# Optimization experiments

Hardware: AMD Instinct MI355X
Metric: run time of the kernel (lower is better)

## Reference

```python
import jax, jax.numpy as jnp
import numpy as np

N = 100000   # nodes
E = 50000    # hyperedges
K = 4        # nodes per hyperedge
D = 128      # out_dim (= in_dim here)
ED = 64      # edge_dim
H = 8        # num_heads


def _build_pairs(seed=0):
    # Sparse equivalent of the incidence-matrix nested loops:
    # for each edge e with member set S, emit ordered pairs (v, e, u) for v,u in S.
    rng = np.random.default_rng(seed)
    cover = rng.permutation(N).reshape(N // K, K)          # guarantees every node owns >=1 pair group
    rand = rng.integers(0, N, size=(E - N // K, K))
    edge_nodes = np.concatenate([cover, rand], axis=0)      # [E, K]
    owners = np.repeat(edge_nodes, K, axis=1).ravel()       # v, repeated K times per edge slot
    pair_u = np.tile(edge_nodes, (1, K)).ravel()            # u, tiled
    pair_e = np.repeat(np.arange(E), K * K)
    return owners.astype(np.int32), pair_e.astype(np.int32), pair_u.astype(np.int32)


def setup_inputs() -> dict:
    key = jax.random.key(0)
    ks = jax.random.split(key, 12)
    owners, pair_e, pair_u = _build_pairs()
    s = 0.05
    return {
        "x": jax.random.normal(ks[0], (N, D), jnp.float32),
        "edge_attr": jax.random.normal(ks[1], (E, ED), jnp.float32),
        "w_lin": jax.random.normal(ks[2], (D, D), jnp.float32) * s,   # self.lin (no bias)
        "w_e": jax.random.normal(ks[3], (ED, D), jnp.float32) * s,    # self.edge_lin (no bias)
        "w_q": jax.random.normal(ks[4], (D, D), jnp.float32) * s,
        "b_q": jax.random.normal(ks[5], (D,), jnp.float32) * s,
        "w_k": jax.random.normal(ks[6], (D, D), jnp.float32) * s,
        "b_k": jax.random.normal(ks[7], (D,), jnp.float32) * s,
        "w_v": jax.random.normal(ks[8], (D, D), jnp.float32) * s,
        "b_v": jax.random.normal(ks[9], (D,), jnp.float32) * s,
        "w_o": jax.random.normal(ks[10], (D, D), jnp.float32) * s,
        "b_o": jax.random.normal(ks[11], (D,), jnp.float32) * s,
        "owners": jnp.asarray(owners),
        "pair_e": jnp.asarray(pair_e),
        "pair_u": jnp.asarray(pair_u),
    }


def reference(x, edge_attr, w_lin, w_e, w_q, b_q, w_k, b_k, w_v, b_v, w_o, b_o, owners, pair_e, pair_u):
    n = x.shape[0]
    d = w_lin.shape[1]
    dh = d // H
    Wh = x @ w_lin                                  # [N, D]
    We = edge_attr @ w_e                            # [E, D]
    # Multi-head single-query attention per node over its (e,u) pair set.
    q = ((Wh @ w_q + b_q) / jnp.sqrt(jnp.asarray(dh, Wh.dtype))).reshape(n, H, dh)
    Wh_u = Wh[pair_u]                               # [P, D] value source (= Wh[u])
    k = ((Wh_u + We[pair_e]) @ w_k + b_k).reshape(-1, H, dh)   # key source = Wh[u] + We[e]
    v = (Wh_u @ w_v + b_v).reshape(-1, H, dh)
    scores = jnp.einsum('phd,phd->ph', q[owners], k)            # [P, H]
    # segmented (ragged) softmax over each node's pair set
    m = jax.ops.segment_max(scores, owners, num_segments=n)
    ex = jnp.exp(scores - m[owners])
    denom = jax.ops.segment_sum(ex, owners, num_segments=n)     # [N, H]
    alpha = ex / denom[owners]                                  # [P, H]
    ctx = jax.ops.segment_sum(alpha[..., None] * v, owners, num_segments=n).reshape(n, d)
    out = ctx @ w_o + b_o
    return jax.nn.relu(out)
```

## Files before the change

kernel.cpp:

```cpp
#include <hip/hip_runtime.h>

#define NN 100000
#define EE 50000
#define GG (EE*4)
#define CAP 24

typedef __attribute__((ext_vector_type(8))) short bf16x8;
typedef __attribute__((ext_vector_type(4))) float f32x4;

__device__ __forceinline__ unsigned short f2bf(float f) {
  union { float f; unsigned int u; } c; c.f = f;
  unsigned int u = c.u;
  u = (u + 0x7fffu + ((u >> 16) & 1u)) >> 16;
  return (unsigned short)u;
}
__device__ __forceinline__ float bf2f(unsigned int lo16) {
  union { unsigned int u; float f; } c; c.u = lo16 << 16;
  return c.f;
}
__device__ __forceinline__ bf16x8 pack8(const float* f) {
  union { bf16x8 v; unsigned int u[4]; } r;
  #pragma unroll
  for (int i = 0; i < 4; ++i)
    r.u[i] = (unsigned int)f2bf(f[2*i]) | ((unsigned int)f2bf(f[2*i+1]) << 16);
  return r.v;
}

struct __align__(8) us4 { unsigned short x, y, z, w; };

__global__ void k_prep(const float* __restrict__ w_lin, const float* __restrict__ w_e,
                       const float* __restrict__ w_q, const float* __restrict__ b_q,
                       const float* __restrict__ w_k, const float* __restrict__ b_k,
                       const float* __restrict__ w_v, const float* __restrict__ b_v,
                       const float* __restrict__ w_o, const float* __restrict__ b_o,
                       unsigned short* __restrict__ WT, unsigned short* __restrict__ WeT,
                       unsigned short* __restrict__ WoT, float* __restrict__ bias384,
                       float* __restrict__ bkB, float* __restrict__ boB) {
  int t = blockIdx.x * 256 + threadIdx.x;
  if (t < 49152) {
    int sel = t >> 14, k = (t >> 7) & 127, nn = t & 127;
    const float* wsel = sel == 0 ? w_q : (sel == 1 ? w_k : w_v);
    float scale = sel == 0 ? 0.25f : 1.0f;
    float s = 0.f;
    for (int d = 0; d < 128; ++d)
      s += w_lin[k*128 + d] * wsel[d*128 + nn];
    WT[(size_t)(sel * 128 + nn) * 128 + k] = f2bf(s * scale);
  } else if (t < 57344) {
    int i = t - 49152, k = i >> 7, nn = i & 127;
    float s = 0.f;
    for (int d = 0; d < 128; ++d)
      s += w_e[k*128 + d] * w_k[d*128 + nn];
    WeT[nn*64 + k] = f2bf(s);
  } else if (t < 73728) {
    int i = t - 57344, k = i >> 7, n = i & 127;
    WoT[n*128 + k] = f2bf(w_o[k*128 + n]);
  } else if (t < 74112) {
    int i = t - 73728;
    bias384[i] = (i < 128) ? b_q[i] * 0.25f : ((i < 256) ? 0.f : b_v[i - 256]);
  } else if (t < 74240) {
    bkB[t - 74112] = b_k[t - 74112];
  } else if (t < 74368) {
    boB[t - 74240] = b_o[t - 74240];
  }
}

__global__ __launch_bounds__(256) void k_qkv(const float* __restrict__ x,
                                             const unsigned short* __restrict__ WT,
                                             const float* __restrict__ bias,
                                             unsigned short* __restrict__ qkv) {
  __shared__ unsigned short As[64 * 136];
  int orig = blockIdx.x;
  int xcd = orig & 7;
  int base = (xcd == 0) ? 0 : 587 + (xcd - 1) * 586;
  int wgid = base + (orig >> 3);
  int row0 = (wgid / 3) * 64;
  int col0 = (wgid % 3) * 128;
  int tid = threadIdx.x;
  #pragma unroll
  for (int it = 0; it < 8; ++it) {
    int i4 = tid + it * 256;
    int r = i4 >> 5, c4 = i4 & 31;
    float4 vv = make_float4(0.f, 0.f, 0.f, 0.f);
    int gr = row0 + r;
    if (gr < NN) vv = *(const float4*)(x + (size_t)gr * 128 + c4 * 4);
    us4 s4 = { f2bf(vv.x), f2bf(vv.y), f2bf(vv.z), f2bf(vv.w) };
    int chunk = c4 >> 1;
    int soff = r * 128 + ((chunk ^ (r & 7)) << 3) + ((c4 & 1) << 2);
    *(us4*)(&As[soff]) = s4;
  }
  __syncthreads();
  int w = tid >> 6, lane = tid & 63, lr = lane & 15, lk = lane >> 4;
  bf16x8 afr[4][4];
  #pragma unroll
  for (int rt = 0; rt < 4; ++rt) {
    int R = rt * 16 + lr;
    #pragma unroll
    for (int kk = 0; kk < 4; ++kk) {
      int chunk = (kk * 4 + lk) ^ (R & 7);
      afr[rt][kk] = *(const bf16x8*)(&As[R * 128 + chunk * 8]);
    }
  }
  f32x4 acc[2][4] = {};
  #pragma unroll
  for (int h = 0; h < 2; ++h) {
    int gcol = col0 + h * 64 + w * 16 + lr;
    const unsigned short* bp = WT + (size_t)gcol * 128 + lk * 8;
    bf16x8 b0 = *(const bf16x8*)(bp);
    bf16x8 b1 = *(const bf16x8*)(bp + 32);
    bf16x8 b2 = *(const bf16x8*)(bp + 64);
    bf16x8 b3 = *(const bf16x8*)(bp + 96);
    #pragma unroll
    for (int rt = 0; rt < 4; ++rt) {
      acc[h][rt] = __builtin_amdgcn_mfma_f32_16x16x32_bf16(afr[rt][0], b0, acc[h][rt], 0, 0, 0);
      acc[h][rt] = __builtin_amdgcn_mfma_f32_16x16x32_bf16(afr[rt][1], b1, acc[h][rt], 0, 0, 0);
      acc[h][rt] = __builtin_amdgcn_mfma_f32_16x16x32_bf16(afr[rt][2], b2, acc[h][rt], 0, 0, 0);
      acc[h][rt] = __builtin_amdgcn_mfma_f32_16x16x32_bf16(afr[rt][3], b3, acc[h][rt], 0, 0, 0);
    }
  }
  __syncthreads();
  #pragma unroll
  for (int h = 0; h < 2; ++h) {
    int colp = h * 64 + w * 16 + lr;
    float b = bias[col0 + colp];
    #pragma unroll
    for (int rt = 0; rt < 4; ++rt) {
      #pragma unroll
      for (int j = 0; j < 4; ++j) {
        As[(rt * 16 + lk * 4 + j) * 136 + colp] = f2bf(acc[h][rt][j] + b);
      }
    }
  }
  __syncthreads();
  int piece = tid & 15, rbase = tid >> 4;
  #pragma unroll
  for (int it = 0; it < 4; ++it) {
    int r = rbase + it * 16;
    int grow = row0 + r;
    if (grow < NN) {
      float4 vv = *(const float4*)(&As[r * 136 + piece * 8]);
      *(float4*)(qkv + (size_t)grow * 384 + col0 + piece * 8) = vv;
    }
  }
}

__global__ __launch_bounds__(256) void k_ke(const float* __restrict__ ea,
                                            const unsigned short* __restrict__ WeT,
                                            const float* __restrict__ bk,
                                            unsigned short* __restrict__ ke) {
  __shared__ unsigned short As[64][72];
  __shared__ unsigned short Bs[64][72];
  int tid = threadIdx.x;
  int row0 = blockIdx.x * 64;
  int col0 = blockIdx.y * 64;
  #pragma unroll
  for (int it = 0; it < 4; ++it) {
    int i4 = tid + it * 256;
    int r = i4 >> 4, c4 = i4 & 15;
    float4 vv = make_float4(0.f, 0.f, 0.f, 0.f);
    int gr = row0 + r;
    if (gr < EE) vv = *(const float4*)(ea + (size_t)gr * 64 + c4 * 4);
    us4 s4 = { f2bf(vv.x), f2bf(vv.y), f2bf(vv.z), f2bf(vv.w) };
    *(us4*)(&As[r][c4 * 4]) = s4;
  }
  #pragma unroll
  for (int it = 0; it < 4; ++it) {
    int i4 = tid + it * 256;
    int r = i4 >> 4, c4 = i4 & 15;
    us4 s4 = *(const us4*)(WeT + (size_t)(col0 + r) * 64 + c4 * 4);
    *(us4*)(&Bs[r][c4 * 4]) = s4;
  }
  __syncthreads();
  int w = tid >> 6, lane = tid & 63, lr = lane & 15, lk = lane >> 4;
  f32x4 acc[4] = {};
  #pragma unroll
  for (int kk = 0; kk < 2; ++kk) {
    int kof = kk * 32 + lk * 8;
    bf16x8 af = *(const bf16x8*)(&As[w * 16 + lr][kof]);
    #pragma unroll
    for (int nt = 0; nt < 4; ++nt) {
      bf16x8 bfrag = *(const bf16x8*)(&Bs[nt * 16 + lr][kof]);
      acc[nt] = __builtin_amdgcn_mfma_f32_16x16x32_bf16(af, bfrag, acc[nt], 0, 0, 0);
    }
  }
  #pragma unroll
  for (int nt = 0; nt < 4; ++nt) {
    int gcol = col0 + nt * 16 + lr;
    float b = bk[gcol];
    #pragma unroll
    for (int j = 0; j < 4; ++j) {
      int grow = row0 + w * 16 + lk * 4 + j;
      if (grow < EE) ke[(size_t)grow * 128 + gcol] = f2bf(acc[nt][j] + b);
    }
  }
}

__global__ void k_bucket(const int* __restrict__ owners, int* __restrict__ cnt,
                         int* __restrict__ glist) {
  int g = blockIdx.x * 256 + threadIdx.x;
  if (g < GG) {
    int v = owners[(size_t)g * 4];
    int p = atomicAdd(cnt + v, 1);
    if (p < CAP) glist[(size_t)v * CAP + p] = g;
  }
}

__global__ __launch_bounds__(256) void k_edge(const unsigned short* __restrict__ qkv,
                                              const unsigned short* __restrict__ ke,
                                              const int* __restrict__ pair_u,
                                              unsigned short* __restrict__ pctx,
                                              float* __restrict__ pden) {
  int e0 = (blockIdx.x * 4 + (threadIdx.x >> 6)) * 4;
  if (e0 >= EE) return;
  int lane = threadIdx.x & 63;
  int m[4][4];
  #pragma unroll
  for (int ee = 0; ee < 4; ++ee)
    #pragma unroll
    for (int j = 0; j < 4; ++j)
      m[ee][j] = __builtin_amdgcn_readfirstlane(pair_u[(size_t)(e0 + ee) * 16 + j]);
  unsigned int kew[4];
  #pragma unroll
  for (int ee = 0; ee < 4; ++ee)
    kew[ee] = *(const unsigned int*)(ke + (size_t)(e0 + ee) * 128 + 2 * lane);
  unsigned int qw[4][4], kw[4][4], vw[4][4];
  #pragma unroll
  for (int ee = 0; ee < 4; ++ee)
    #pragma unroll
    for (int j = 0; j < 4; ++j) {
      const unsigned short* r = qkv + (size_t)m[ee][j] * 384 + 2 * lane;
      qw[ee][j] = *(const unsigned int*)r;
      kw[ee][j] = *(const unsigned int*)(r + 128);
      vw[ee][j] = *(const unsigned int*)(r + 256);
    }
  #pragma unroll
  for (int ee = 0; ee < 4; ++ee) {
    float e0f = bf2f(kew[ee] & 0xffffu), e1f = bf2f(kew[ee] >> 16);
    float qa[4][2], ka[4][2], va[4][2];
    #pragma unroll
    for (int j = 0; j < 4; ++j) {
      qa[j][0] = bf2f(qw[ee][j] & 0xffffu);        qa[j][1] = bf2f(qw[ee][j] >> 16);
      ka[j][0] = bf2f(kw[ee][j] & 0xffffu) + e0f;  ka[j][1] = bf2f(kw[ee][j] >> 16) + e1f;
      va[j][0] = bf2f(vw[ee][j] & 0xffffu);        va[j][1] = bf2f(vw[ee][j] >> 16);
    }
    #pragma unroll
    for (int i = 0; i < 4; ++i) {
      float c0 = 0.f, c1 = 0.f, ds = 0.f;
      #pragma unroll
      for (int j = 0; j < 4; ++j) {
        float sc = qa[i][0] * ka[j][0] + qa[i][1] * ka[j][1];
        sc += __shfl_xor(sc, 1);
        sc += __shfl_xor(sc, 2);
        sc += __shfl_xor(sc, 4);
        float ex = __expf(sc);
        c0 += ex * va[j][0];
        c1 += ex * va[j][1];
        ds += ex;
      }
      int slot = (e0 + ee) * 4 + i;
      unsigned int packed = (unsigned int)f2bf(c0) | ((unsigned int)f2bf(c1) << 16);
      *(unsigned int*)(pctx + (size_t)slot * 128 + 2 * lane) = packed;
      if ((lane & 7) == 0) pden[(size_t)slot * 8 + (lane >> 3)] = ds;
    }
  }
}

__global__ __launch_bounds__(256) void k_out(const unsigned short* __restrict__ pctx,
                                             const float* __restrict__ pden,
                                             const int* __restrict__ cnt,
                                             const int* __restrict__ glist,
                                             const unsigned short* __restrict__ WoT,
                                             const float* __restrict__ bo,
                                             float* __restrict__ out) {
  int wid = blockIdx.x * 4 + (threadIdx.x >> 6);
  if (wid >= NN / 32) return;
  int lane = threadIdx.x & 63, lr = lane & 15, lk = lane >> 4;
  int rowA = wid * 32 + lr, rowB = rowA + 16;
  float aA[4][8], aB[4][8];
  float dsA[4] = { 0.f, 0.f, 0.f, 0.f }, dsB[4] = { 0.f, 0.f, 0.f, 0.f };
  #pragma unroll
  for (int kk = 0; kk < 4; ++kk)
    #pragma unroll
    for (int i = 0; i < 8; ++i) { aA[kk][i] = 0.f; aB[kk][i] = 0.f; }
  int cA = cnt[rowA]; if (cA > CAP) cA = CAP;
  int cB = cnt[rowB]; if (cB > CAP) cB = CAP;
  int iA = 0, iB = 0;
  for (;;) {
    bool doA = iA < cA, doB = iB < cB;
    if (!__any((int)(doA || doB))) break;
    if (doA) {
      int sl = glist[(size_t)rowA * CAP + iA];
      const unsigned short* pr = pctx + (size_t)sl * 128 + lk * 8;
      const float* dp = pden + (size_t)sl * 8 + (lk >> 1);
      #pragma unroll
      for (int kk = 0; kk < 4; ++kk) {
        uint4 v = *(const uint4*)(pr + kk * 32);
        aA[kk][0] += bf2f(v.x & 0xffffu); aA[kk][1] += bf2f(v.x >> 16);
        aA[kk][2] += bf2f(v.y & 0xffffu); aA[kk][3] += bf2f(v.y >> 16);
        aA[kk][4] += bf2f(v.z & 0xffffu); aA[kk][5] += bf2f(v.z >> 16);
        aA[kk][6] += bf2f(v.w & 0xffffu); aA[kk][7] += bf2f(v.w >> 16);
        dsA[kk] += dp[kk * 2];
      }
      ++iA;
    }
    if (doB) {
      int sl = glist[(size_t)rowB * CAP + iB];
      const unsigned short* pr = pctx + (size_t)sl * 128 + lk * 8;
      const float* dp = pden + (size_t)sl * 8 + (lk >> 1);
      #pragma unroll
      for (int kk = 0; kk < 4; ++kk) {
        uint4 v = *(const uint4*)(pr + kk * 32);
        aB[kk][0] += bf2f(v.x & 0xffffu); aB[kk][1] += bf2f(v.x >> 16);
        aB[kk][2] += bf2f(v.y & 0xffffu); aB[kk][3] += bf2f(v.y >> 16);
        aB[kk][4] += bf2f(v.z & 0xffffu); aB[kk][5] += bf2f(v.z >> 16);
        aB[kk][6] += bf2f(v.w & 0xffffu); aB[kk][7] += bf2f(v.w >> 16);
        dsB[kk] += dp[kk * 2];
      }
      ++iB;
    }
  }
  bf16x8 abfA[4], abfB[4];
  #pragma unroll
  for (int kk = 0; kk < 4; ++kk) {
    float invA = dsA[kk] > 0.f ? 1.0f / dsA[kk] : 0.f;
    float invB = dsB[kk] > 0.f ? 1.0f / dsB[kk] : 0.f;
    float fA[8], fB[8];
    #pragma unroll
    for (int i = 0; i < 8; ++i) { fA[i] = aA[kk][i] * invA; fB[i] = aB[kk][i] * invB; }
    abfA[kk] = pack8(fA);
    abfB[kk] = pack8(fB);
  }
  #pragma unroll
  for (int ct = 0; ct < 8; ++ct) {
    const unsigned short* wp = WoT + (size_t)(ct * 16 + lr) * 128 + lk * 8;
    bf16x8 w0 = *(const bf16x8*)(wp);
    bf16x8 w1 = *(const bf16x8*)(wp + 32);
    bf16x8 w2 = *(const bf16x8*)(wp + 64);
    bf16x8 w3 = *(const bf16x8*)(wp + 96);
    f32x4 accA = {}, accB = {};
    accA = __builtin_amdgcn_mfma_f32_16x16x32_bf16(w0, abfA[0], accA, 0, 0, 0);
    accA = __builtin_amdgcn_mfma_f32_16x16x32_bf16(w1, abfA[1], accA, 0, 0, 0);
    accA = __builtin_amdgcn_mfma_f32_16x16x32_bf16(w2, abfA[2], accA, 0, 0, 0);
    accA = __builtin_amdgcn_mfma_f32_16x16x32_bf16(w3, abfA[3], accA, 0, 0, 0);
    accB = __builtin_amdgcn_mfma_f32_16x16x32_bf16(w0, abfB[0], accB, 0, 0, 0);
    accB = __builtin_amdgcn_mfma_f32_16x16x32_bf16(w1, abfB[1], accB, 0, 0, 0);
    accB = __builtin_amdgcn_mfma_f32_16x16x32_bf16(w2, abfB[2], accB, 0, 0, 0);
    accB = __builtin_amdgcn_mfma_f32_16x16x32_bf16(w3, abfB[3], accB, 0, 0, 0);
    float4 bb = *(const float4*)(bo + ct * 16 + lk * 4);
    float4 oA, oB;
    oA.x = fmaxf(accA[0] + bb.x, 0.f); oA.y = fmaxf(accA[1] + bb.y, 0.f);
    oA.z = fmaxf(accA[2] + bb.z, 0.f); oA.w = fmaxf(accA[3] + bb.w, 0.f);
    oB.x = fmaxf(accB[0] + bb.x, 0.f); oB.y = fmaxf(accB[1] + bb.y, 0.f);
    oB.z = fmaxf(accB[2] + bb.z, 0.f); oB.w = fmaxf(accB[3] + bb.w, 0.f);
    *(float4*)(out + (size_t)rowA * 128 + ct * 16 + lk * 4) = oA;
    *(float4*)(out + (size_t)rowB * 128 + ct * 16 + lk * 4) = oB;
  }
}

extern "C" void kernel_launch(void* const* d_in, const int* in_sizes, int n_in,
                              void* d_out, int out_size, void* d_ws, size_t ws_size,
                              hipStream_t stream) {
  const float* x      = (const float*)d_in[0];
  const float* ea     = (const float*)d_in[1];
  const float* w_lin  = (const float*)d_in[2];
  const float* w_e    = (const float*)d_in[3];
  const float* w_q    = (const float*)d_in[4];
  const float* b_q    = (const float*)d_in[5];
  const float* w_k    = (const float*)d_in[6];
  const float* b_k    = (const float*)d_in[7];
  const float* w_v    = (const float*)d_in[8];
  const float* b_v    = (const float*)d_in[9];
  const float* w_o    = (const float*)d_in[10];
  const float* b_o    = (const float*)d_in[11];
  const int* owners   = (const int*)d_in[12];
  const int* pair_u   = (const int*)d_in[14];
  float* out = (float*)d_out;

  char* base = (char*)d_ws;
  size_t o = 0;
  auto alloc = [&](size_t b) {
    void* p = base + o;
    o = (o + b + 255) & ~(size_t)255;
    return p;
  };
  unsigned short* WT      = (unsigned short*)alloc((size_t)384 * 128 * 2);
  unsigned short* WeT     = (unsigned short*)alloc((size_t)128 * 64 * 2);
  unsigned short* WoT     = (unsigned short*)alloc((size_t)128 * 128 * 2);
  float* bias384          = (float*)alloc(384 * 4);
  float* bkB              = (float*)alloc(128 * 4);
  float* boB              = (float*)alloc(128 * 4);
  unsigned short* qkv     = (unsigned short*)alloc((size_t)NN * 384 * 2);
  unsigned short* keb     = (unsigned short*)alloc((size_t)EE * 128 * 2);
  int* cnt                = (int*)alloc((size_t)NN * 4);
  int* glist              = (int*)alloc((size_t)NN * CAP * 4);
  unsigned short* pctx    = (unsigned short*)alloc((size_t)GG * 128 * 2);
  float* pden             = (float*)alloc((size_t)GG * 8 * 4);

  hipMemsetAsync(cnt, 0, (size_t)NN * 4, stream);

  k_prep<<<291, 256, 0, stream>>>(w_lin, w_e, w_q, b_q, w_k, b_k, w_v, b_v, w_o, b_o,
                                  WT, WeT, WoT, bias384, bkB, boB);
  k_qkv<<<4689, 256, 0, stream>>>(x, WT, bias384, qkv);
  k_ke<<<dim3(782, 2), 256, 0, stream>>>(ea, WeT, bkB, keb);
  k_bucket<<<782, 256, 0, stream>>>(owners, cnt, glist);
  k_edge<<<3125, 256, 0, stream>>>(qkv, keb, pair_u, pctx, pden);
  k_out<<<782, 256, 0, stream>>>(pctx, pden, cnt, glist, WoT, boB, out);
}
```

Before: 171.1 us.

## Merge QKV, edge-key and bucketing kernels into one launch; compute all QKV columns per block

Folds the three independent mid-stage kernels (QKV projection, edge-key projection, owner bucketing) into one kernel that dispatches on block index. This removes two launches and the serialization between them. The QKV part now makes each block handle all 384 output columns for its 64 rows, so the x tile is converted and staged in shared memory once instead of three times. The XCD-aware block remapping is dropped, and each QKV block now does three times the work, which may hurt load balance or L2 locality.

```diff
diff --git a/kernel.cpp b/kernel.cpp
--- a/kernel.cpp
+++ b/kernel.cpp
@@ -4,6 +4,10 @@
 #define EE 50000
 #define GG (EE*4)
 #define CAP 24
+
+#define QKV_BLOCKS 1563
+#define KE_BLOCKS  1564
+#define BKT_BLOCKS 782
 
 typedef __attribute__((ext_vector_type(8))) short bf16x8;
 typedef __attribute__((ext_vector_type(4))) float f32x4;
@@ -64,143 +68,145 @@
   }
 }
 
-__global__ __launch_bounds__(256) void k_qkv(const float* __restrict__ x,
+__global__ __launch_bounds__(256) void k_mid(const float* __restrict__ x,
                                              const unsigned short* __restrict__ WT,
                                              const float* __restrict__ bias,
-                                             unsigned short* __restrict__ qkv) {
-  __shared__ unsigned short As[64 * 136];
-  int orig = blockIdx.x;
-  int xcd = orig & 7;
-  int base = (xcd == 0) ? 0 : 587 + (xcd - 1) * 586;
-  int wgid = base + (orig >> 3);
-  int row0 = (wgid / 3) * 64;
-  int col0 = (wgid % 3) * 128;
+                                             unsigned short* __restrict__ qkv,
+                                             const float* __restrict__ ea,
+                                             const unsigned short* __restrict__ WeT,
+                                             const float* __restrict__ bk,
+                                             unsigned short* __restrict__ ke,
+                                             const int* __restrict__ owners,
+                                             int* __restrict__ cnt,
+                                             int* __restrict__ glist) {
+  __shared__ unsigned short lds[64 * 144];
+  int bid = blockIdx.x;
   int tid = threadIdx.x;
-  #pragma unroll
-  for (int it = 0; it < 8; ++it) {
-    int i4 = tid + it * 256;
-    int r = i4 >> 5, c4 = i4 & 31;
-    float4 vv = make_float4(0.f, 0.f, 0.f, 0.f);
-    int gr = row0 + r;
-    if (gr < NN) vv = *(const float4*)(x + (size_t)gr * 128 + c4 * 4);
-    us4 s4 = { f2bf(vv.x), f2bf(vv.y), f2bf(vv.z), f2bf(vv.w) };
-    int chunk = c4 >> 1;
-    int soff = r * 128 + ((chunk ^ (r & 7)) << 3) + ((c4 & 1) << 2);
-    *(us4*)(&As[soff]) = s4;
-  }
-  __syncthreads();
-  int w = tid >> 6, lane = tid & 63, lr = lane & 15, lk = lane >> 4;
-  bf16x8 afr[4][4];
-  #pragma unroll
-  for (int rt = 0; rt < 4; ++rt) {
-    int R = rt * 16 + lr;
-    #pragma unroll
-    for (int kk = 0; kk < 4; ++kk) {
-      int chunk = (kk * 4 + lk) ^ (R & 7);
-      afr[rt][kk] = *(const bf16x8*)(&As[R * 128 + chunk * 8]);
-    }
-  }
-  f32x4 acc[2][4] = {};
-  #pragma unroll
-  for (int h = 0; h < 2; ++h) {
-    int gcol = col0 + h * 64 + w * 16 + lr;
-    const unsigned short* bp = WT + (size_t)gcol * 128 + lk * 8;
-    bf16x8 b0 = *(const bf16x8*)(bp);
-    bf16x8 b1 = *(const bf16x8*)(bp + 32);
-    bf16x8 b2 = *(const bf16x8*)(bp + 64);
-    bf16x8 b3 = *(const bf16x8*)(bp + 96);
+
+  if (bid < QKV_BLOCKS) {
+    unsigned short* As = lds;
+    int row0 = bid * 64;
+    #pragma unroll
+    for (int it = 0; it < 8; ++it) {
+      int i4 = tid + it * 256;
+      int r = i4 >> 5, c4 = i4 & 31;
+      float4 vv = make_float4(0.f, 0.f, 0.f, 0.f);
+      int gr = row0 + r;
+      if (gr < NN) vv = *(const float4*)(x + (size_t)gr * 128 + c4 * 4);
+      us4 s4 = { f2bf(vv.x), f2bf(vv.y), f2bf(vv.z), f2bf(vv.w) };
+      int chunk = c4 >> 1;
+      int soff = r * 128 + ((chunk ^ (r & 7)) << 3) + ((c4 & 1) << 2);
+      *(us4*)(&As[soff]) = s4;
+    }
+    __syncthreads();
+    int w = tid >> 6, lane = tid & 63, lr = lane & 15, lk = lane >> 4;
+    bf16x8 afr[4][4];
     #pragma unroll
     for (int rt = 0; rt < 4; ++rt) {
-      acc[h][rt] = __builtin_amdgcn_mfma_f32_16x16x32_bf16(afr[rt][0], b0, acc[h][rt], 0, 0, 0);
-      acc[h][rt] = __builtin_amdgcn_mfma_f32_16x16x32_bf16(afr[rt][1], b1, acc[h][rt], 0, 0, 0);
-      acc[h][rt] = __builtin_amdgcn_mfma_f32_16x16x32_bf16(afr[rt][2], b2, acc[h][rt], 0, 0, 0);
-      acc[h][rt] = __builtin_amdgcn_mfma_f32_16x16x32_bf16(afr[rt][3], b3, acc[h][rt], 0, 0, 0);
-    }
-  }
-  __syncthreads();
-  #pragma unroll
-  for (int h = 0; h < 2; ++h) {
-    int colp = h * 64 + w * 16 + lr;
-    float b = bias[col0 + colp];
-    #pragma unroll
-    for (int rt = 0; rt < 4; ++rt) {
+      int R = rt * 16 + lr;
+      #pragma unroll
+      for (int kk = 0; kk < 4; ++kk) {
+        int chunk = (kk * 4 + lk) ^ (R & 7);
+        afr[rt][kk] = *(const bf16x8*)(&As[R * 128 + chunk * 8]);
+      }
+    }
+    #pragma unroll
+    for (int p = 0; p < 3; ++p) {
+      f32x4 acc[2][4] = {};
+      #pragma unroll
+      for (int h = 0; h < 2; ++h) {
+        int gcol = p * 128 + h * 64 + w * 16 + lr;
+        const unsigned short* bp = WT + (size_t)gcol * 128 + lk * 8;
+        bf16x8 b0 = *(const bf16x8*)(bp);
+        bf16x8 b1 = *(const bf16x8*)(bp + 32);
+        bf16x8 b2 = *(const bf16x8*)(bp + 64);
+        bf16x8 b3 = *(const bf16x8*)(bp + 96);
+        #pragma unroll
+        for (int rt = 0; rt < 4; ++rt) {
+          acc[h][rt] = __builtin_amdgcn_mfma_f32_16x16x32_bf16(afr[rt][0], b0, acc[h][rt], 0, 0, 0);
+          acc[h][rt] = __builtin_amdgcn_mfma_f32_16x16x32_bf16(afr[rt][1], b1, acc[h][rt], 0, 0, 0);
+          acc[h][rt] = __builtin_amdgcn_mfma_f32_16x16x32_bf16(afr[rt][2], b2, acc[h][rt], 0, 0, 0);
+          acc[h][rt] = __builtin_amdgcn_mfma_f32_16x16x32_bf16(afr[rt][3], b3, acc[h][rt], 0, 0, 0);
+        }
+      }
+      __syncthreads();
+      #pragma unroll
+      for (int h = 0; h < 2; ++h) {
+        int colp = h * 64 + w * 16 + lr;
+        float b = bias[p * 128 + colp];
+        #pragma unroll
+        for (int rt = 0; rt < 4; ++rt) {
+          #pragma unroll
+          for (int j = 0; j < 4; ++j) {
+            As[(rt * 16 + lk * 4 + j) * 136 + colp] = f2bf(acc[h][rt][j] + b);
+          }
+        }
+      }
+      __syncthreads();
+      int piece = tid & 15, rbase = tid >> 4;
+      #pragma unroll
+      for (int it = 0; it < 4; ++it) {
+        int r = rbase + it * 16;
+        int grow = row0 + r;
+        if (grow < NN) {
+          float4 vv = *(const float4*)(&As[r * 136 + piece * 8]);
+          *(float4*)(qkv + (size_t)grow * 384 + p * 128 + piece * 8) = vv;
+        }
+      }
+    }
+  } else if (bid < QKV_BLOCKS + KE_BLOCKS) {
+    int idx = bid - QKV_BLOCKS;
+    int row0 = (idx % 782) * 64;
+    int col0 = (idx / 782) * 64;
+    unsigned short* As = lds;
+    unsigned short* Bs = lds + 64 * 72;
+    #pragma unroll
+    for (int it = 0; it < 4; ++it) {
+      int i4 = tid + it * 256;
+      int r = i4 >> 4, c4 = i4 & 15;
+      float4 vv = make_float4(0.f, 0.f, 0.f, 0.f);
+      int gr = row0 + r;
+      if (gr < EE) vv = *(const float4*)(ea + (size_t)gr * 64 + c4 * 4);
+      us4 s4 = { f2bf(vv.x), f2bf(vv.y), f2bf(vv.z), f2bf(vv.w) };
+      *(us4*)(&As[r * 72 + c4 * 4]) = s4;
+    }
+    #pragma unroll
+    for (int it = 0; it < 4; ++it) {
+      int i4 = tid + it * 256;
+      int r = i4 >> 4, c4 = i4 & 15;
+      us4 s4 = *(const us4*)(WeT + (size_t)(col0 + r) * 64 + c4 * 4);
+      *(us4*)(&Bs[r * 72 + c4 * 4]) = s4;
+    }
+    __syncthreads();
+    int w = tid >> 6, lane = tid & 63, lr = lane & 15, lk = lane >> 4;
+    f32x4 acc[4] = {};
+    #pragma unroll
+    for (int kk = 0; kk < 2; ++kk) {
+      int kof = kk * 32 + lk * 8;
+      bf16x8 af = *(const bf16x8*)(&As[(w * 16 + lr) * 72 + kof]);
+      #pragma unroll
+      for (int nt = 0; nt < 4; ++nt) {
+        bf16x8 bfrag = *(const bf16x8*)(&Bs[(nt * 16 + lr) * 72 + kof]);
+        acc[nt] = __builtin_amdgcn_mfma_f32_16x16x32_bf16(af, bfrag, acc[nt], 0, 0, 0);
+      }
+    }
+    #pragma unroll
+    for (int nt = 0; nt < 4; ++nt) {
+      int gcol = col0 + nt * 16 + lr;
+      float b = bk[gcol];
       #pragma unroll
       for (int j = 0; j < 4; ++j) {
-        As[(rt * 16 + lk * 4 + j) * 136 + colp] = f2bf(acc[h][rt][j] + b);
-      }
-    }
-  }
-  __syncthreads();
-  int piece = tid & 15, rbase = tid >> 4;
-  #pragma unroll
-  for (int it = 0; it < 4; ++it) {
-    int r = rbase + it * 16;
-    int grow = row0 + r;
-    if (grow < NN) {
-      float4 vv = *(const float4*)(&As[r * 136 + piece * 8]);
-      *(float4*)(qkv + (size_t)grow * 384 + col0 + piece * 8) = vv;
-    }
-  }
-}
-
-__global__ __launch_bounds__(256) void k_ke(const float* __restrict__ ea,
-                                            const unsigned short* __restrict__ WeT,
-                                            const float* __restrict__ bk,
-                                            unsigned short* __restrict__ ke) {
-  __shared__ unsigned short As[64][72];
-  __shared__ unsigned short Bs[64][72];
-  int tid = threadIdx.x;
-  int row0 = blockIdx.x * 64;
-  int col0 = blockIdx.y * 64;
-  #pragma unroll
-  for (int it = 0; it < 4; ++it) {
-    int i4 = tid + it * 256;
-    int r = i4 >> 4, c4 = i4 & 15;
-    float4 vv = make_float4(0.f, 0.f, 0.f, 0.f);
-    int gr = row0 + r;
-    if (gr < EE) vv = *(const float4*)(ea + (size_t)gr * 64 + c4 * 4);
-    us4 s4 = { f2bf(vv.x), f2bf(vv.y), f2bf(vv.z), f2bf(vv.w) };
-    *(us4*)(&As[r][c4 * 4]) = s4;
-  }
-  #pragma unroll
-  for (int it = 0; it < 4; ++it) {
-    int i4 = tid + it * 256;
-    int r = i4 >> 4, c4 = i4 & 15;
-    us4 s4 = *(const us4*)(WeT + (size_t)(col0 + r) * 64 + c4 * 4);
-    *(us4*)(&Bs[r][c4 * 4]) = s4;
-  }
-  __syncthreads();
-  int w = tid >> 6, lane = tid & 63, lr = lane & 15, lk = lane >> 4;
-  f32x4 acc[4] = {};
-  #pragma unroll
-  for (int kk = 0; kk < 2; ++kk) {
-    int kof = kk * 32 + lk * 8;
-    bf16x8 af = *(const bf16x8*)(&As[w * 16 + lr][kof]);
-    #pragma unroll
-    for (int nt = 0; nt < 4; ++nt) {
-      bf16x8 bfrag = *(const bf16x8*)(&Bs[nt * 16 + lr][kof]);
-      acc[nt] = __builtin_amdgcn_mfma_f32_16x16x32_bf16(af, bfrag, acc[nt], 0, 0, 0);
-    }
-  }
-  #pragma unroll
-  for (int nt = 0; nt < 4; ++nt) {
-    int gcol = col0 + nt * 16 + lr;
-    float b = bk[gcol];
-    #pragma unroll
-    for (int j = 0; j < 4; ++j) {
-      int grow = row0 + w * 16 + lk * 4 + j;
-      if (grow < EE) ke[(size_t)grow * 128 + gcol] = f2bf(acc[nt][j] + b);
-    }
-  }
-}
-
-__global__ void k_bucket(const int* __restrict__ owners, int* __restrict__ cnt,
-                         int* __restrict__ glist) {
-  int g = blockIdx.x * 256 + threadIdx.x;
-  if (g < GG) {
-    int v = owners[(size_t)g * 4];
-    int p = atomicAdd(cnt + v, 1);
-    if (p < CAP) glist[(size_t)v * CAP + p] = g;
+        int grow = row0 + w * 16 + lk * 4 + j;
+        if (grow < EE) ke[(size_t)grow * 128 + gcol] = f2bf(acc[nt][j] + b);
+      }
+    }
+  } else {
+    int g = (bid - QKV_BLOCKS - KE_BLOCKS) * 256 + tid;
+    if (g < GG) {
+      int v = owners[(size_t)g * 4];
+      int p = atomicAdd(cnt + v, 1);
+      if (p < CAP) glist[(size_t)v * CAP + p] = g;
+    }
   }
 }
 
@@ -399,9 +405,8 @@
 
   k_prep<<<291, 256, 0, stream>>>(w_lin, w_e, w_q, b_q, w_k, b_k, w_v, b_v, w_o, b_o,
                                   WT, WeT, WoT, bias384, bkB, boB);
-  k_qkv<<<4689, 256, 0, stream>>>(x, WT, bias384, qkv);
-  k_ke<<<dim3(782, 2), 256, 0, stream>>>(ea, WeT, bkB, keb);
-  k_bucket<<<782, 256, 0, stream>>>(owners, cnt, glist);
+  k_mid<<<QKV_BLOCKS + KE_BLOCKS + BKT_BLOCKS, 256, 0, stream>>>(
+      x, WT, bias384, qkv, ea, WeT, bkB, keb, owners, cnt, glist);
   k_edge<<<3125, 256, 0, stream>>>(qkv, keb, pair_u, pctx, pden);
   k_out<<<782, 256, 0, stream>>>(pctx, pden, cnt, glist, WoT, boB, out);
 }
```

Result: faster. 152.4 us (median of 2 runs) (-10.9%).
